# Performance work log

Measured on AMD Instinct MI355X. Metric: run time of the kernel, lower is better.

The kernel has to match this reference:

```python
import jax, jax.numpy as jnp
import numpy as np

DIM = 512

def setup_inputs() -> dict:
    key = jax.random.key(0)
    k1, k2, k3, k4 = jax.random.split(key, 4)
    c = jax.random.normal(k1, (32, 2048, DIM), dtype=jnp.float32)
    q = jax.random.normal(k2, (32, 512, DIM), dtype=jnp.float32)
    # nn.Linear(dim, dim): weight (out,in), bias (out,)
    bound = 1.0 / np.sqrt(DIM)
    W = jax.random.uniform(k3, (DIM, DIM), dtype=jnp.float32, minval=-bound, maxval=bound)
    b = jax.random.uniform(k4, (DIM,), dtype=jnp.float32, minval=-bound, maxval=bound)
    return {"c": c, "q": q, "W": W, "b": b}

def reference(c, q, W, b):
    # Shared linear + ReLU projection for both context and question
    c_feat = jax.nn.relu(jnp.einsum('bcd,ed->bce', c, W) + b)  # (B, c_len, dim)
    q_feat = jax.nn.relu(jnp.einsum('bqd,ed->bqe', q, W) + b)  # (B, q_len, dim)
    # Unscaled attention scores (B, c_len, q_len), softmax over q_len
    attn = jax.nn.softmax(jnp.einsum('bce,bqe->bcq', c_feat, q_feat), axis=-1)
    # Weighted sum of raw q vectors
    mix = jnp.einsum('bcq,bqd->bcd', attn, q)
    return mix
```

## Files before the change

kernel.cpp:

```cpp
#include <hip/hip_runtime.h>


#define BATCH 32
#define CL    2048
#define QL    512
#define DIM   512
#define CT    64

typedef _Float16 f16x8 __attribute__((ext_vector_type(8)));
typedef _Float16 f16x4 __attribute__((ext_vector_type(4)));
typedef float    f32x4 __attribute__((ext_vector_type(4)));

#define LDP 72

__global__ void k_shuf_f16(const _Float16* __restrict__ in, _Float16* __restrict__ out) {
    size_t g = (size_t)blockIdx.x * 256 + threadIdx.x;
    int rt = (int)(g >> 10), ks = (int)(g >> 6) & 15, l = (int)g & 63;
    const _Float16* src = in + ((size_t)(rt * 16 + (l & 15))) * 512 + ks * 32 + (l >> 4) * 8;
    *(uint4*)(out + g * 8) = *(const uint4*)src;
}

__global__ void k_shuf_f32(const float* __restrict__ in, _Float16* __restrict__ out) {
    size_t g = (size_t)blockIdx.x * 256 + threadIdx.x;
    int rt = (int)(g >> 10), ks = (int)(g >> 6) & 15, l = (int)g & 63;
    const float* src = in + ((size_t)(rt * 16 + (l & 15))) * 512 + ks * 32 + (l >> 4) * 8;
    float4 v0 = *(const float4*)src;
    float4 v1 = *(const float4*)(src + 4);
    f16x8 h = {(_Float16)v0.x, (_Float16)v0.y, (_Float16)v0.z, (_Float16)v0.w,
               (_Float16)v1.x, (_Float16)v1.y, (_Float16)v1.z, (_Float16)v1.w};
    *(f16x8*)(out + g * 8) = h;
}

__global__ void k_prep_qt(const float* __restrict__ q, _Float16* __restrict__ qT) {
    __shared__ _Float16 t[64][65];
    int b  = blockIdx.x;
    int jt = blockIdx.y;
    int dt = blockIdx.z;
    const float* src = q + ((size_t)b * QL + jt * 64) * DIM + dt * 64;
    int r0 = threadIdx.x >> 6;
    int cc = threadIdx.x & 63;
#pragma unroll
    for (int p = 0; p < 16; ++p) {
        int r = r0 + p * 4;
        t[r][cc] = (_Float16)src[(size_t)r * DIM + cc];
    }
    __syncthreads();
    _Float16* dst = qT + ((size_t)b * DIM + dt * 64) * QL + jt * 64;
#pragma unroll
    for (int p = 0; p < 16; ++p) {
        int r = r0 + p * 4;
        dst[(size_t)r * QL + cc] = t[cc][r];
    }
}

__global__ __launch_bounds__(256)
__attribute__((amdgpu_waves_per_eu(3)))
void k_proj(const float* __restrict__ X, const _Float16* __restrict__ WhS,
            const float* __restrict__ bias, _Float16* __restrict__ Y) {
    __shared__ __align__(16) _Float16 Ah[128 * LDP];
    int m0 = blockIdx.x * 128;
    int n0 = blockIdx.y * 128;
    int tid = threadIdx.x;
    int w = tid >> 6, lane = tid & 63;
    int col = lane & 15, quad = lane >> 4;
    int wm = (w >> 1) * 64, wn = (w & 1) * 64;
    int et0 = (n0 + wn) >> 4;

    f32x4 acc[4][4];
#pragma unroll
    for (int it = 0; it < 4; ++it)
#pragma unroll
        for (int jt = 0; jt < 4; ++jt) acc[it][jt] = (f32x4){0.f, 0.f, 0.f, 0.f};

    for (int kc = 0; kc < 8; ++kc) {
#pragma unroll
        for (int p = 0; p < 8; ++p) {
            int s = tid + p * 256;
            int r = s >> 4, c4 = (s & 15) * 4;
            float4 v = *(const float4*)(X + (size_t)(m0 + r) * DIM + kc * 64 + c4);
            f16x4 h = {(_Float16)v.x, (_Float16)v.y, (_Float16)v.z, (_Float16)v.w};
            *(f16x4*)&Ah[r * LDP + c4] = h;
        }
        __syncthreads();
#pragma unroll
        for (int kc2 = 0; kc2 < 2; ++kc2) {
            int ks = kc * 2 + kc2;
            f16x8 af[4], bf[4];
#pragma unroll
            for (int it = 0; it < 4; ++it)
                af[it] = *(const f16x8*)&Ah[(wm + it * 16 + col) * LDP + kc2 * 32 + quad * 8];
#pragma unroll
            for (int jt = 0; jt < 4; ++jt)
                bf[jt] = *(const f16x8*)(WhS + (((size_t)(et0 + jt) * 16 + ks) * 64 + lane) * 8);
#pragma unroll
            for (int it = 0; it < 4; ++it)
#pragma unroll
                for (int jt = 0; jt < 4; ++jt)
                    acc[it][jt] = __builtin_amdgcn_mfma_f32_16x16x32_f16(af[it], bf[jt], acc[it][jt], 0, 0, 0);
        }
        __syncthreads();
    }
#pragma unroll
    for (int jt = 0; jt < 4; ++jt) {
        int e = n0 + wn + jt * 16 + col;
        float bv = bias[e];
#pragma unroll
        for (int it = 0; it < 4; ++it)
#pragma unroll
            for (int r = 0; r < 4; ++r) {
                int row = m0 + wm + it * 16 + quad * 4 + r;
                Y[(size_t)row * DIM + e] = (_Float16)fmaxf(acc[it][jt][r] + bv, 0.f);
            }
    }
}

__global__ __launch_bounds__(512)
__attribute__((amdgpu_waves_per_eu(4)))
void k_fused(const float* __restrict__ C, const _Float16* __restrict__ WhS,
             const float* __restrict__ bias,
             const _Float16* __restrict__ qfS, const _Float16* __restrict__ qTS,
             float* __restrict__ out) {
    __shared__ __align__(16) _Float16 At[CT * DIM];
    __shared__ float redmax[8][CT];
    __shared__ float redsum[8][CT];

    int bx   = blockIdx.x;
    int xcd  = bx & 7;
    int slot = bx >> 3;
    int b    = xcd + 8 * (slot >> 5);
    int c0   = (slot & 31) * CT;

    int tid   = threadIdx.x;
    int w     = tid >> 6, lane = tid & 63;
    int col   = lane & 15, quad = lane >> 4;
    int obase = w * 64;
    int cs    = col & 7;

    const float* cb = C + ((size_t)b * CL + c0) * DIM;
#pragma unroll
    for (int p = 0; p < 8; ++p) {
        int s = tid + p * 512;
        int r = s >> 6, u = s & 63;
        const float* src = cb + (size_t)r * DIM + u * 8;
        float4 v0 = *(const float4*)src;
        float4 v1 = *(const float4*)(src + 4);
        f16x8 h = {(_Float16)v0.x, (_Float16)v0.y, (_Float16)v0.z, (_Float16)v0.w,
                   (_Float16)v1.x, (_Float16)v1.y, (_Float16)v1.z, (_Float16)v1.w};
        *(f16x8*)&At[r * DIM + ((u ^ (r & 7)) << 3)] = h;
    }
    __syncthreads();

    f32x4 acc[4][4];

#pragma unroll
    for (int it = 0; it < 4; ++it)
#pragma unroll
        for (int jt = 0; jt < 4; ++jt) acc[it][jt] = (f32x4){0.f, 0.f, 0.f, 0.f};
    {
        int et0 = w * 4;
#pragma unroll 2
        for (int kc = 0; kc < 16; ++kc) {
            int ku = kc * 4 + quad;
            f16x8 af[4], bf[4];
#pragma unroll
            for (int it = 0; it < 4; ++it)
                af[it] = *(const f16x8*)&At[(it * 16 + col) * DIM + ((ku ^ cs) << 3)];
#pragma unroll
            for (int jt = 0; jt < 4; ++jt)
                bf[jt] = *(const f16x8*)(WhS + (((size_t)(et0 + jt) * 16 + kc) * 64 + lane) * 8);
#pragma unroll
            for (int it = 0; it < 4; ++it)
#pragma unroll
                for (int jt = 0; jt < 4; ++jt)
                    acc[it][jt] = __builtin_amdgcn_mfma_f32_16x16x32_f16(af[it], bf[jt], acc[it][jt], 0, 0, 0);
        }
    }
    __syncthreads();
#pragma unroll
    for (int jt = 0; jt < 4; ++jt) {
        int e = obase + jt * 16 + col;
        float bv = bias[e];
        int ue = e >> 3, we = e & 7;
#pragma unroll
        for (int it = 0; it < 4; ++it)
#pragma unroll
            for (int r = 0; r < 4; ++r) {
                int m = it * 16 + quad * 4 + r;
                At[m * DIM + (((ue ^ (m & 7)) << 3) | we)] =
                    (_Float16)fmaxf(acc[it][jt][r] + bv, 0.f);
            }
    }
    __syncthreads();

#pragma unroll
    for (int it = 0; it < 4; ++it)
#pragma unroll
        for (int jt = 0; jt < 4; ++jt) acc[it][jt] = (f32x4){0.f, 0.f, 0.f, 0.f};
    int rt0 = b * 32 + w * 4;
#pragma unroll 2
    for (int kc = 0; kc < 16; ++kc) {
        int ku = kc * 4 + quad;
        f16x8 af[4], bf[4];
#pragma unroll
        for (int it = 0; it < 4; ++it)
            af[it] = *(const f16x8*)&At[(it * 16 + col) * DIM + ((ku ^ cs) << 3)];
#pragma unroll
        for (int jt = 0; jt < 4; ++jt)
            bf[jt] = *(const f16x8*)(qfS + (((size_t)(rt0 + jt) * 16 + kc) * 64 + lane) * 8);
#pragma unroll
        for (int it = 0; it < 4; ++it)
#pragma unroll
            for (int jt = 0; jt < 4; ++jt)
                acc[it][jt] = __builtin_amdgcn_mfma_f32_16x16x32_f16(af[it], bf[jt], acc[it][jt], 0, 0, 0);
    }

    float sm[4][4];
#pragma unroll
    for (int it = 0; it < 4; ++it)
#pragma unroll
        for (int r = 0; r < 4; ++r) {
            float m = -1e30f;
#pragma unroll
            for (int jt = 0; jt < 4; ++jt) m = fmaxf(m, acc[it][jt][r]);
            m = fmaxf(m, __shfl_xor(m, 1));
            m = fmaxf(m, __shfl_xor(m, 2));
            m = fmaxf(m, __shfl_xor(m, 4));
            m = fmaxf(m, __shfl_xor(m, 8));
            sm[it][r] = m;
        }
    if (col == 0) {
#pragma unroll
        for (int it = 0; it < 4; ++it)
#pragma unroll
            for (int r = 0; r < 4; ++r) redmax[w][it * 16 + quad * 4 + r] = sm[it][r];
    }
    __syncthreads();
#pragma unroll
    for (int it = 0; it < 4; ++it)
#pragma unroll
        for (int r = 0; r < 4; ++r) {
            int i = it * 16 + quad * 4 + r;
            float gm = redmax[0][i];
#pragma unroll
            for (int v = 1; v < 8; ++v) gm = fmaxf(gm, redmax[v][i]);
            float s = 0.f;
#pragma unroll
            for (int jt = 0; jt < 4; ++jt) {
                float e = __expf(acc[it][jt][r] - gm);
                acc[it][jt][r] = e;
                s += e;
            }
            s += __shfl_xor(s, 1);
            s += __shfl_xor(s, 2);
            s += __shfl_xor(s, 4);
            s += __shfl_xor(s, 8);
            sm[it][r] = s;
        }
    if (col == 0) {
#pragma unroll
        for (int it = 0; it < 4; ++it)
#pragma unroll
            for (int r = 0; r < 4; ++r) redsum[w][it * 16 + quad * 4 + r] = sm[it][r];
    }
    __syncthreads();
#pragma unroll
    for (int it = 0; it < 4; ++it)
#pragma unroll
        for (int r = 0; r < 4; ++r) {
            int i = it * 16 + quad * 4 + r;
            float tot = 0.f;
#pragma unroll
            for (int v = 0; v < 8; ++v) tot += redsum[v][i];
            float inv = 1.f / tot;
#pragma unroll
            for (int jt = 0; jt < 4; ++jt) {
                int j = obase + jt * 16 + col;
                int uj = j >> 3, wj = j & 7;
                At[i * DIM + (((uj ^ (i & 7)) << 3) | wj)] =
                    (_Float16)(acc[it][jt][r] * inv);
            }
        }
    __syncthreads();

#pragma unroll
    for (int it = 0; it < 4; ++it)
#pragma unroll
        for (int jt = 0; jt < 4; ++jt) acc[it][jt] = (f32x4){0.f, 0.f, 0.f, 0.f};
#pragma unroll 2
    for (int kc = 0; kc < 16; ++kc) {
        int ku = kc * 4 + quad;
        f16x8 af[4], bf[4];
#pragma unroll
        for (int it = 0; it < 4; ++it)
            af[it] = *(const f16x8*)&At[(it * 16 + col) * DIM + ((ku ^ cs) << 3)];
#pragma unroll
        for (int dt = 0; dt < 4; ++dt)
            bf[dt] = *(const f16x8*)(qTS + (((size_t)(rt0 + dt) * 16 + kc) * 64 + lane) * 8);
#pragma unroll
        for (int it = 0; it < 4; ++it)
#pragma unroll
            for (int dt = 0; dt < 4; ++dt)
                acc[it][dt] = __builtin_amdgcn_mfma_f32_16x16x32_f16(af[it], bf[dt], acc[it][dt], 0, 0, 0);
    }

#pragma unroll
    for (int dt = 0; dt < 4; ++dt) {
        int d = obase + dt * 16 + col;
#pragma unroll
        for (int it = 0; it < 4; ++it)
#pragma unroll
            for (int r = 0; r < 4; ++r) {
                int m = it * 16 + quad * 4 + r;
                out[((size_t)b * CL + c0 + m) * DIM + d] = acc[it][dt][r];
            }
    }
}

extern "C" void kernel_launch(void* const* d_in, const int* in_sizes, int n_in,
                              void* d_out, int out_size, void* d_ws, size_t ws_size,
                              hipStream_t stream) {
    const float* c    = (const float*)d_in[0];
    const float* q    = (const float*)d_in[1];
    const float* W    = (const float*)d_in[2];
    const float* bias = (const float*)d_in[3];
    float* out = (float*)d_out;

    char* ws = (char*)d_ws;
    _Float16* WhS = (_Float16*)ws;
    _Float16* qfS = (_Float16*)(ws + (1u << 19));
    _Float16* qTS = (_Float16*)(ws + (1u << 19) + (1u << 24));
    _Float16* qf  = (_Float16*)(ws + (1u << 19) + 2u * (1u << 24));
    _Float16* qT  = (_Float16*)(ws + (1u << 19) + 3u * (1u << 24));

    k_shuf_f32<<<128, 256, 0, stream>>>(W, WhS);
    k_proj<<<dim3(BATCH * QL / 128, 4), 256, 0, stream>>>(q, WhS, bias, qf);
    k_shuf_f16<<<4096, 256, 0, stream>>>(qf, qfS);
    k_prep_qt<<<dim3(BATCH, QL / 64, DIM / 64), 256, 0, stream>>>(q, qT);
    k_shuf_f16<<<4096, 256, 0, stream>>>(qT, qTS);
    k_fused<<<BATCH * (CL / CT), 512, 0, stream>>>(c, WhS, bias, qfS, qTS, out);
}
```

Measured before the change: 467.7 us.

## Write fragment layout directly, widen fused kernel warp tiles, stage output via LDS

The projection and transpose kernels now write straight into the MFMA fragment-shuffled layout, so the two extra shuffle kernels and their intermediate buffers go away. The fused kernel drops from 512 to 256 threads, and each wave covers 128 output columns (a 4x8 tile). The global B-fragment loads are double-buffered across k steps. The final output is staged through swizzled LDS so it can be written with coalesced vector stores. This cuts launches and global traffic and raises fragment reuse per wave, at the cost of higher register pressure and lower occupancy (waves_per_eu 2).

```diff
diff --git a/kernel.cpp b/kernel.cpp
--- a/kernel.cpp
+++ b/kernel.cpp
@@ -13,11 +13,8 @@
 
 #define LDP 72
 
-__global__ void k_shuf_f16(const _Float16* __restrict__ in, _Float16* __restrict__ out) {
-    size_t g = (size_t)blockIdx.x * 256 + threadIdx.x;
-    int rt = (int)(g >> 10), ks = (int)(g >> 6) & 15, l = (int)g & 63;
-    const _Float16* src = in + ((size_t)(rt * 16 + (l & 15))) * 512 + ks * 32 + (l >> 4) * 8;
-    *(uint4*)(out + g * 8) = *(const uint4*)src;
+__device__ __forceinline__ size_t frag_off(int m, int e) {
+    return (((size_t)(m >> 4) * 16 + (e >> 5)) * 64 + ((e >> 3) & 3) * 16 + (m & 15)) * 8 + (e & 7);
 }
 
 __global__ void k_shuf_f32(const float* __restrict__ in, _Float16* __restrict__ out) {
@@ -31,7 +28,7 @@
     *(f16x8*)(out + g * 8) = h;
 }
 
-__global__ void k_prep_qt(const float* __restrict__ q, _Float16* __restrict__ qT) {
+__global__ void k_prep_qt(const float* __restrict__ q, _Float16* __restrict__ qTS) {
     __shared__ _Float16 t[64][65];
     int b  = blockIdx.x;
     int jt = blockIdx.y;
@@ -45,18 +42,19 @@
         t[r][cc] = (_Float16)src[(size_t)r * DIM + cc];
     }
     __syncthreads();
-    _Float16* dst = qT + ((size_t)b * DIM + dt * 64) * QL + jt * 64;
 #pragma unroll
     for (int p = 0; p < 16; ++p) {
         int r = r0 + p * 4;
-        dst[(size_t)r * QL + cc] = t[cc][r];
+        int d = dt * 64 + r;
+        int j = jt * 64 + cc;
+        qTS[frag_off(b * 512 + d, j)] = t[cc][r];
     }
 }
 
 __global__ __launch_bounds__(256)
 __attribute__((amdgpu_waves_per_eu(3)))
-void k_proj(const float* __restrict__ X, const _Float16* __restrict__ WhS,
-            const float* __restrict__ bias, _Float16* __restrict__ Y) {
+void k_projS(const float* __restrict__ X, const _Float16* __restrict__ WhS,
+             const float* __restrict__ bias, _Float16* __restrict__ Y) {
     __shared__ __align__(16) _Float16 Ah[128 * LDP];
     int m0 = blockIdx.x * 128;
     int n0 = blockIdx.y * 128;
@@ -108,21 +106,59 @@
         for (int it = 0; it < 4; ++it)
 #pragma unroll
             for (int r = 0; r < 4; ++r) {
-                int row = m0 + wm + it * 16 + quad * 4 + r;
-                Y[(size_t)row * DIM + e] = (_Float16)fmaxf(acc[it][jt][r] + bv, 0.f);
-            }
-    }
-}
-
-__global__ __launch_bounds__(512)
-__attribute__((amdgpu_waves_per_eu(4)))
+                int m = m0 + wm + it * 16 + quad * 4 + r;
+                Y[frag_off(m, e)] = (_Float16)fmaxf(acc[it][jt][r] + bv, 0.f);
+            }
+    }
+}
+
+#define AFREAD(AF, KC)                                                        \
+    { int ku_ = (KC) * 4 + quad;                                              \
+      _Pragma("unroll")                                                       \
+      for (int it = 0; it < 4; ++it)                                          \
+          AF[it] = *(const f16x8*)&At[(it * 16 + col) * DIM + ((ku_ ^ cs) << 3)]; }
+
+#define MFMAS(AF, BF)                                                         \
+    _Pragma("unroll")                                                         \
+    for (int it = 0; it < 4; ++it)                                            \
+        _Pragma("unroll")                                                     \
+        for (int jt = 0; jt < 8; ++jt)                                        \
+            acc[it][jt] = __builtin_amdgcn_mfma_f32_16x16x32_f16(AF[it], BF[jt], acc[it][jt], 0, 0, 0);
+
+#define LOADB(DST, BASE, RT0, KC)                                             \
+    _Pragma("unroll")                                                         \
+    for (int jt = 0; jt < 8; ++jt)                                            \
+        DST[jt] = *(const f16x8*)((BASE) + (((size_t)(((RT0) + jt) * 16 + (KC))) * 64 + lane) * 8);
+
+#define PHASE(BASE, RT0)                                                      \
+    { f16x8 ba_[8], bb_[8], af_[4];                                           \
+      LOADB(ba_, BASE, RT0, 0)                                                \
+      _Pragma("unroll")                                                       \
+      for (int kk = 0; kk < 8; ++kk) {                                        \
+          AFREAD(af_, kk * 2)                                                 \
+          LOADB(bb_, BASE, RT0, kk * 2 + 1)                                   \
+          MFMAS(af_, ba_)                                                     \
+          AFREAD(af_, kk * 2 + 1)                                             \
+          if (kk < 7) { LOADB(ba_, BASE, RT0, kk * 2 + 2) }                   \
+          MFMAS(af_, bb_)                                                     \
+      } }
+
+#define ZEROACC                                                               \
+    _Pragma("unroll")                                                         \
+    for (int it = 0; it < 4; ++it)                                            \
+        _Pragma("unroll")                                                     \
+        for (int jt = 0; jt < 8; ++jt) acc[it][jt] = (f32x4){0.f, 0.f, 0.f, 0.f};
+
+__global__ __launch_bounds__(256)
+__attribute__((amdgpu_waves_per_eu(2)))
 void k_fused(const float* __restrict__ C, const _Float16* __restrict__ WhS,
              const float* __restrict__ bias,
              const _Float16* __restrict__ qfS, const _Float16* __restrict__ qTS,
              float* __restrict__ out) {
     __shared__ __align__(16) _Float16 At[CT * DIM];
-    __shared__ float redmax[8][CT];
-    __shared__ float redsum[8][CT];
+    __shared__ float redmax[4][CT];
+    __shared__ float redsum[4][CT];
+    float* fAt = (float*)At;
 
     int bx   = blockIdx.x;
     int xcd  = bx & 7;
@@ -133,13 +169,14 @@
     int tid   = threadIdx.x;
     int w     = tid >> 6, lane = tid & 63;
     int col   = lane & 15, quad = lane >> 4;
-    int obase = w * 64;
+    int obase = w * 128;
     int cs    = col & 7;
+    int rt0q  = b * 32 + w * 8;
 
     const float* cb = C + ((size_t)b * CL + c0) * DIM;
 #pragma unroll
-    for (int p = 0; p < 8; ++p) {
-        int s = tid + p * 512;
+    for (int p = 0; p < 16; ++p) {
+        int s = tid + p * 256;
         int r = s >> 6, u = s & 63;
         const float* src = cb + (size_t)r * DIM + u * 8;
         float4 v0 = *(const float4*)src;
@@ -150,34 +187,13 @@
     }
     __syncthreads();
 
-    f32x4 acc[4][4];
-
-#pragma unroll
-    for (int it = 0; it < 4; ++it)
-#pragma unroll
-        for (int jt = 0; jt < 4; ++jt) acc[it][jt] = (f32x4){0.f, 0.f, 0.f, 0.f};
-    {
-        int et0 = w * 4;
-#pragma unroll 2
-        for (int kc = 0; kc < 16; ++kc) {
-            int ku = kc * 4 + quad;
-            f16x8 af[4], bf[4];
-#pragma unroll
-            for (int it = 0; it < 4; ++it)
-                af[it] = *(const f16x8*)&At[(it * 16 + col) * DIM + ((ku ^ cs) << 3)];
-#pragma unroll
-            for (int jt = 0; jt < 4; ++jt)
-                bf[jt] = *(const f16x8*)(WhS + (((size_t)(et0 + jt) * 16 + kc) * 64 + lane) * 8);
-#pragma unroll
-            for (int it = 0; it < 4; ++it)
-#pragma unroll
-                for (int jt = 0; jt < 4; ++jt)
-                    acc[it][jt] = __builtin_amdgcn_mfma_f32_16x16x32_f16(af[it], bf[jt], acc[it][jt], 0, 0, 0);
-        }
-    }
-    __syncthreads();
-#pragma unroll
-    for (int jt = 0; jt < 4; ++jt) {
+    f32x4 acc[4][8];
+
+    ZEROACC
+    PHASE(WhS, w * 8)
+    __syncthreads();
+#pragma unroll
+    for (int jt = 0; jt < 8; ++jt) {
         int e = obase + jt * 16 + col;
         float bv = bias[e];
         int ue = e >> 3, we = e & 7;
@@ -192,27 +208,8 @@
     }
     __syncthreads();
 
-#pragma unroll
-    for (int it = 0; it < 4; ++it)
-#pragma unroll
-        for (int jt = 0; jt < 4; ++jt) acc[it][jt] = (f32x4){0.f, 0.f, 0.f, 0.f};
-    int rt0 = b * 32 + w * 4;
-#pragma unroll 2
-    for (int kc = 0; kc < 16; ++kc) {
-        int ku = kc * 4 + quad;
-        f16x8 af[4], bf[4];
-#pragma unroll
-        for (int it = 0; it < 4; ++it)
-            af[it] = *(const f16x8*)&At[(it * 16 + col) * DIM + ((ku ^ cs) << 3)];
-#pragma unroll
-        for (int jt = 0; jt < 4; ++jt)
-            bf[jt] = *(const f16x8*)(qfS + (((size_t)(rt0 + jt) * 16 + kc) * 64 + lane) * 8);
-#pragma unroll
-        for (int it = 0; it < 4; ++it)
-#pragma unroll
-            for (int jt = 0; jt < 4; ++jt)
-                acc[it][jt] = __builtin_amdgcn_mfma_f32_16x16x32_f16(af[it], bf[jt], acc[it][jt], 0, 0, 0);
-    }
+    ZEROACC
+    PHASE(qfS, rt0q)
 
     float sm[4][4];
 #pragma unroll
@@ -221,7 +218,7 @@
         for (int r = 0; r < 4; ++r) {
             float m = -1e30f;
 #pragma unroll
-            for (int jt = 0; jt < 4; ++jt) m = fmaxf(m, acc[it][jt][r]);
+            for (int jt = 0; jt < 8; ++jt) m = fmaxf(m, acc[it][jt][r]);
             m = fmaxf(m, __shfl_xor(m, 1));
             m = fmaxf(m, __shfl_xor(m, 2));
             m = fmaxf(m, __shfl_xor(m, 4));
@@ -240,12 +237,11 @@
 #pragma unroll
         for (int r = 0; r < 4; ++r) {
             int i = it * 16 + quad * 4 + r;
-            float gm = redmax[0][i];
-#pragma unroll
-            for (int v = 1; v < 8; ++v) gm = fmaxf(gm, redmax[v][i]);
+            float gm = fmaxf(fmaxf(redmax[0][i], redmax[1][i]),
+                             fmaxf(redmax[2][i], redmax[3][i]));
             float s = 0.f;
 #pragma unroll
-            for (int jt = 0; jt < 4; ++jt) {
+            for (int jt = 0; jt < 8; ++jt) {
                 float e = __expf(acc[it][jt][r] - gm);
                 acc[it][jt][r] = e;
                 s += e;
@@ -268,12 +264,10 @@
 #pragma unroll
         for (int r = 0; r < 4; ++r) {
             int i = it * 16 + quad * 4 + r;
-            float tot = 0.f;
-#pragma unroll
-            for (int v = 0; v < 8; ++v) tot += redsum[v][i];
+            float tot = redsum[0][i] + redsum[1][i] + redsum[2][i] + redsum[3][i];
             float inv = 1.f / tot;
 #pragma unroll
-            for (int jt = 0; jt < 4; ++jt) {
+            for (int jt = 0; jt < 8; ++jt) {
                 int j = obase + jt * 16 + col;
                 int uj = j >> 3, wj = j & 7;
                 At[i * DIM + (((uj ^ (i & 7)) << 3) | wj)] =
@@ -282,37 +276,40 @@
         }
     __syncthreads();
 
-#pragma unroll
-    for (int it = 0; it < 4; ++it)
-#pragma unroll
-        for (int jt = 0; jt < 4; ++jt) acc[it][jt] = (f32x4){0.f, 0.f, 0.f, 0.f};
-#pragma unroll 2
-    for (int kc = 0; kc < 16; ++kc) {
-        int ku = kc * 4 + quad;
-        f16x8 af[4], bf[4];
-#pragma unroll
-        for (int it = 0; it < 4; ++it)
-            af[it] = *(const f16x8*)&At[(it * 16 + col) * DIM + ((ku ^ cs) << 3)];
-#pragma unroll
-        for (int dt = 0; dt < 4; ++dt)
-            bf[dt] = *(const f16x8*)(qTS + (((size_t)(rt0 + dt) * 16 + kc) * 64 + lane) * 8);
-#pragma unroll
-        for (int it = 0; it < 4; ++it)
-#pragma unroll
-            for (int dt = 0; dt < 4; ++dt)
-                acc[it][dt] = __builtin_amdgcn_mfma_f32_16x16x32_f16(af[it], bf[dt], acc[it][dt], 0, 0, 0);
-    }
-
-#pragma unroll
-    for (int dt = 0; dt < 4; ++dt) {
-        int d = obase + dt * 16 + col;
-#pragma unroll
-        for (int it = 0; it < 4; ++it)
-#pragma unroll
-            for (int r = 0; r < 4; ++r) {
-                int m = it * 16 + quad * 4 + r;
-                out[((size_t)b * CL + c0 + m) * DIM + d] = acc[it][dt][r];
-            }
+    ZEROACC
+    PHASE(qTS, rt0q)
+    __syncthreads();
+
+#pragma unroll
+    for (int h = 0; h < 2; ++h) {
+#pragma unroll
+        for (int it = 2 * h; it < 2 * h + 2; ++it)
+#pragma unroll
+            for (int jt = 0; jt < 8; ++jt) {
+                int d = obase + jt * 16 + col;
+#pragma unroll
+                for (int r = 0; r < 4; ++r) {
+                    int lr = (it & 1) * 16 + quad * 4 + r;
+                    int key = ((lr >> 2) & 3) << 4;
+                    fAt[lr * DIM + (d ^ key)] = acc[it][jt][r];
+                }
+            }
+        __syncthreads();
+        const float* outrow0 = out + ((size_t)b * CL + c0 + h * 32) * DIM;
+#pragma unroll
+        for (int p = 0; p < 8; ++p) {
+            int o   = p * 2048 + tid * 8;
+            int row = o >> 9;
+            int d0  = o & 511;
+            int key = ((row >> 2) & 3) << 4;
+            int idx = row * DIM + (d0 ^ key);
+            f32x4 v0 = *(const f32x4*)&fAt[idx];
+            f32x4 v1 = *(const f32x4*)&fAt[idx + 4];
+            float* dst = (float*)outrow0 + (size_t)row * DIM + d0;
+            *(f32x4*)dst = v0;
+            *(f32x4*)(dst + 4) = v1;
+        }
+        if (h == 0) __syncthreads();
     }
 }
 
@@ -329,13 +326,9 @@
     _Float16* WhS = (_Float16*)ws;
     _Float16* qfS = (_Float16*)(ws + (1u << 19));
     _Float16* qTS = (_Float16*)(ws + (1u << 19) + (1u << 24));
-    _Float16* qf  = (_Float16*)(ws + (1u << 19) + 2u * (1u << 24));
-    _Float16* qT  = (_Float16*)(ws + (1u << 19) + 3u * (1u << 24));
 
     k_shuf_f32<<<128, 256, 0, stream>>>(W, WhS);
-    k_proj<<<dim3(BATCH * QL / 128, 4), 256, 0, stream>>>(q, WhS, bias, qf);
-    k_shuf_f16<<<4096, 256, 0, stream>>>(qf, qfS);
-    k_prep_qt<<<dim3(BATCH, QL / 64, DIM / 64), 256, 0, stream>>>(q, qT);
-    k_shuf_f16<<<4096, 256, 0, stream>>>(qT, qTS);
-    k_fused<<<BATCH * (CL / CT), 512, 0, stream>>>(c, WhS, bias, qfS, qTS, out);
-}
+    k_projS<<<dim3(BATCH * QL / 128, 4), 256, 0, stream>>>(q, WhS, bias, qfS);
+    k_prep_qt<<<dim3(BATCH, QL / 64, DIM / 64), 256, 0, stream>>>(q, qTS);
+    k_fused<<<BATCH * (CL / CT), 256, 0, stream>>>(c, WhS, bias, qfS, qTS, out);
+}
```

New measurement: 560.8 us. +19.9%, slower.
